# Kernel optimization log

Measured on AMD Instinct MI355X. Metric: run time of the kernel, lower is better.

## Reference

```python
import jax, jax.numpy as jnp
import numpy as np

N = 10000      # atoms
E = 160000     # edges (avg degree 16)
C = 64         # hidden_channels
R = 32         # num_rbf
CUTOFF = 5.0   # cutoff_upper (cutoff_lower = 0)


def setup_inputs() -> dict:
    key = jax.random.key(0)
    ks = jax.random.split(key, 12)
    X = jax.random.normal(ks[0], (N, C, 3, 3), jnp.float32) * 0.1
    edge_index = jax.random.randint(ks[1], (2, E), 0, N, dtype=jnp.int32)
    edge_weight = jax.random.uniform(ks[2], (E,), jnp.float32, minval=0.1, maxval=CUTOFF)
    edge_attr = jax.random.normal(ks[3], (E, R), jnp.float32)
    # scalar MLP: R -> C -> 2C -> 3C (weights stored [in, out] so y = x @ W + b)
    W_s1 = jax.random.normal(ks[4], (R, C), jnp.float32) / np.sqrt(R)
    b_s1 = jnp.zeros((C,), jnp.float32)
    W_s2 = jax.random.normal(ks[5], (C, 2 * C), jnp.float32) / np.sqrt(C)
    b_s2 = jnp.zeros((2 * C,), jnp.float32)
    W_s3 = jax.random.normal(ks[6], (2 * C, 3 * C), jnp.float32) / np.sqrt(2 * C)
    b_s3 = jnp.zeros((3 * C,), jnp.float32)
    # 6 channel-mixing linears (bias-free), stored [in, out]
    Wt = jax.random.normal(ks[7], (6, C, C), jnp.float32) / np.sqrt(C)
    return dict(X=X, edge_index=edge_index, edge_weight=edge_weight, edge_attr=edge_attr,
                W_s1=W_s1, b_s1=b_s1, W_s2=W_s2, b_s2=b_s2, W_s3=W_s3, b_s3=b_s3, Wt=Wt)


def _decompose(T):
    # irreducible decomposition of [..., 3, 3]
    eye = jnp.eye(3, dtype=T.dtype)
    I = (jnp.trace(T, axis1=-2, axis2=-1) / 3.0)[..., None, None] * eye
    A = 0.5 * (T - jnp.swapaxes(T, -2, -1))
    S = 0.5 * (T + jnp.swapaxes(T, -2, -1)) - I
    return I, A, S


def _tnorm(T):
    # Frobenius norm^2 over last two dims -> [..., C]
    return jnp.sum(T * T, axis=(-2, -1))


def _chan_lin(T, W):
    # linear over channel dim: [n, k, 3, 3] x [k, l] -> [n, l, 3, 3]
    return jnp.einsum('nkij,kl->nlij', T, W)


def reference(X, edge_index, edge_weight, edge_attr,
              W_s1, b_s1, W_s2, b_s2, W_s3, b_s3, Wt):
    act = jax.nn.silu
    # CosineCutoff with cutoff_lower == 0
    Cw = 0.5 * (jnp.cos(edge_weight * (jnp.pi / CUTOFF)) + 1.0)
    Cw = Cw * (edge_weight < CUTOFF).astype(X.dtype)

    # scalar edge MLP -> per-edge per-channel factors for I/A/S
    a = act(edge_attr @ W_s1 + b_s1)
    a = act(a @ W_s2 + b_s2)
    a = act(a @ W_s3 + b_s3)                       # [E, 3C]
    a = (a * Cw[:, None]).reshape(-1, C, 3)        # [E, C, 3]

    # normalize node tensors
    Xn = X / (_tnorm(X) + 1.0)[..., None, None]
    I, A, S = _decompose(Xn)
    I = _chan_lin(I, Wt[0])
    A = _chan_lin(A, Wt[1])
    S = _chan_lin(S, Wt[2])
    Y = I + A + S

    src, dst = edge_index[0], edge_index[1]

    def mp(factor, T):
        # gather -> weight -> scatter-add   factor: [E, C, 1, 1]
        msg = factor * T[dst]
        return jax.ops.segment_sum(msg, src, num_segments=N)

    msg = (mp(a[:, :, 0, None, None], I)
           + mp(a[:, :, 1, None, None], A)
           + mp(a[:, :, 2, None, None], S))

    # O(3) equivariance group
    M = jnp.matmul(msg, Y) + jnp.matmul(Y, msg)
    I2, A2, S2 = _decompose(M)
    normp1 = (_tnorm(I2 + A2 + S2) + 1.0)[..., None, None]
    I2 = _chan_lin(I2 / normp1, Wt[3])
    A2 = _chan_lin(A2 / normp1, Wt[4])
    S2 = _chan_lin(S2 / normp1, Wt[5])
    dX = I2 + A2 + S2
    return Xn + dX + jnp.matmul(dX, dX)
```

## Files before the change

kernel.cpp:

```cpp
#include <hip/hip_runtime.h>
#include <math.h>

#define C 64
#define R 32
#define CUTOFF 5.0f
#define PI_F 3.14159265358979323846f

typedef __attribute__((ext_vector_type(8))) short short8b;
typedef __attribute__((ext_vector_type(4))) short short4b;
typedef __attribute__((ext_vector_type(4))) float f32x4;

__device__ __forceinline__ float silu(float x) { return x / (1.0f + __expf(-x)); }

__device__ __forceinline__ unsigned short f2bfu(float x) {
  unsigned u = __builtin_bit_cast(unsigned, x);
  u += 0x7FFF + ((u >> 16) & 1);
  return (unsigned short)(u >> 16);
}
__device__ __forceinline__ float bflo(unsigned u) {
  return __builtin_bit_cast(float, u << 16);
}
__device__ __forceinline__ float bfhi(unsigned u) {
  return __builtin_bit_cast(float, u & 0xffff0000u);
}
__device__ __forceinline__ unsigned pk2(float a, float b) {
  return (unsigned)f2bfu(a) | ((unsigned)f2bfu(b) << 16);
}

__global__ __launch_bounds__(256) void k_misc(
    const int* __restrict__ ei, int* __restrict__ deg, int E, int histB,
    const float* __restrict__ W1, const float* __restrict__ W2,
    const float* __restrict__ W3, unsigned short* __restrict__ Wf,
    const float* __restrict__ X, const float* __restrict__ Wt,
    float* __restrict__ Xn, float* __restrict__ nf32,
    unsigned* __restrict__ nfh, int N) {
  __shared__ float comps[4][C][12];
  const int bid = blockIdx.x;
  if (bid < histB) {
    int e = bid * 256 + threadIdx.x;
    if (e < E) atomicAdd(&deg[ei[e]], 1);
    return;
  }
  if (bid < histB + 136) {
    int id = (bid - histB) * 256 + threadIdx.x;
    if (id >= 34816) return;
    int i, l, t;
    if (id < 2048) {
      i = id & 7; l = (id >> 3) & 63; t = id >> 9;
      int nt = t % 4, ks = t / 4;
      int k = ks * 32 + ((l >> 4) << 2) + (i & 3) + ((i >> 2) << 4);
      int n = nt * 16 + (l & 15);
      Wf[id] = f2bfu(W1[(size_t)k * 64 + n]);
    } else if (id < 10240) {
      int id2 = id - 2048;
      i = id2 & 7; l = (id2 >> 3) & 63; t = id2 >> 9;
      int nt = t % 8, ks = t / 8;
      int k = ks * 32 + ((l >> 4) << 2) + (i & 3) + ((i >> 2) << 4);
      int n = nt * 16 + (l & 15);
      Wf[id] = f2bfu(W2[(size_t)k * 128 + n]);
    } else {
      int id2 = id - 10240;
      i = id2 & 7; l = (id2 >> 3) & 63; t = id2 >> 9;
      int nt = t % 12, ks = t / 12;
      int k = ks * 32 + ((l >> 4) << 2) + (i & 3) + ((i >> 2) << 4);
      int nperm = nt * 16 + (l & 15);
      int norig = (nperm & 63) * 3 + (nperm >> 6);
      Wf[id] = f2bfu(W3[(size_t)k * 192 + norig]);
    }
    return;
  }
  const int ln = threadIdx.x >> 6;
  const int c  = threadIdx.x & 63;
  const int node = (bid - histB - 136) * 4 + ln;
  if (node < N) {
    const float* xp = X + ((size_t)node * C + c) * 9;
    float x[9]; float nrm = 0.f;
#pragma unroll
    for (int j = 0; j < 9; j++) { x[j] = xp[j]; nrm += x[j] * x[j]; }
    const float inv = 1.0f / (nrm + 1.0f);
#pragma unroll
    for (int j = 0; j < 9; j++) x[j] *= inv;
    float* xnp = Xn + (size_t)node * 576 + c;
#pragma unroll
    for (int j = 0; j < 9; j++) xnp[j * 64] = x[j];
    const float tr3 = (x[0] + x[4] + x[8]) * (1.f / 3.f);
    float* cp = comps[ln][c];
    cp[0] = tr3;
    cp[1] = 0.5f * (x[1] - x[3]);
    cp[2] = 0.5f * (x[2] - x[6]);
    cp[3] = 0.5f * (x[5] - x[7]);
    cp[4] = x[0] - tr3;
    cp[5] = x[4] - tr3;
    cp[6] = x[8] - tr3;
    cp[7] = 0.5f * (x[1] + x[3]);
    cp[8] = 0.5f * (x[2] + x[6]);
    cp[9] = 0.5f * (x[5] + x[7]);
  }
  __syncthreads();
  if (node < N) {
    const float* W0 = Wt;
    const float* Wt1 = Wt + C * C;
    const float* Wt2 = Wt + 2 * C * C;
    float o[10];
#pragma unroll
    for (int j = 0; j < 10; j++) o[j] = 0.f;
    for (int k = 0; k < C; k++) {
      const float w0 = W0[k * C + c];
      const float w1 = Wt1[k * C + c];
      const float w2 = Wt2[k * C + c];
      const float4* cq = (const float4*)comps[ln][k];
      float4 q0 = cq[0], q1 = cq[1];
      float2 q2 = *(const float2*)(comps[ln][k] + 8);
      o[0] += q0.x * w0;
      o[1] += q0.y * w1; o[2] += q0.z * w1; o[3] += q0.w * w1;
      o[4] += q1.x * w2; o[5] += q1.y * w2; o[6] += q1.z * w2;
      o[7] += q1.w * w2; o[8] += q2.x * w2; o[9] += q2.y * w2;
    }
    float* np_ = nf32 + (size_t)node * 768 + c * 12;
    *(float4*)np_       = make_float4(o[0], o[1], o[2], o[3]);
    *(float4*)(np_ + 4) = make_float4(o[4], o[5], o[6], o[7]);
    *(float4*)(np_ + 8) = make_float4(o[8], o[9], 0.f, 0.f);
    unsigned ui = f2bfu(o[0]);
    unsigned* hp = nfh + (size_t)node * 384 + c * 6;
    *(uint2*)hp       = make_uint2(ui | ((unsigned)f2bfu(o[4]) << 16),
                                   ui | ((unsigned)f2bfu(o[5]) << 16));
    *(uint2*)(hp + 2) = make_uint2(ui | ((unsigned)f2bfu(o[6]) << 16),
                                   pk2(o[1], o[7]));
    *(uint2*)(hp + 4) = make_uint2(pk2(o[2], o[8]), pk2(o[3], o[9]));
  }
}

__global__ __launch_bounds__(1024) void k_scan(const int* __restrict__ deg,
                                               int* __restrict__ off,
                                               int* __restrict__ cur, int N) {
  __shared__ int sums[1024];
  const int t = threadIdx.x;
  const int L = (N + 1023) / 1024;
  const int base = t * L;
  int s = 0;
  for (int j = 0; j < L; j++) if (base + j < N) s += deg[base + j];
  sums[t] = s;
  __syncthreads();
  for (int d = 1; d < 1024; d <<= 1) {
    int v = (t >= d) ? sums[t - d] : 0;
    __syncthreads();
    sums[t] += v;
    __syncthreads();
  }
  int run = (t > 0) ? sums[t - 1] : 0;
  for (int j = 0; j < L; j++) {
    int i = base + j;
    if (i < N) { off[i] = run; run += deg[i]; cur[i] = 0; }
  }
  if (t == 1023) off[N] = sums[1023];
}

__global__ __launch_bounds__(256) void k_mlp(
    const float* __restrict__ ew, const float* __restrict__ ea,
    const int* __restrict__ ei,
    const float* __restrict__ b1, const float* __restrict__ b2,
    const float* __restrict__ b3, const unsigned short* __restrict__ Wf,
    const int* __restrict__ off, int* __restrict__ cur,
    int* __restrict__ dlist, unsigned short* __restrict__ fa, int E) {
  __shared__ __align__(16) unsigned short attrB[64][40];
  __shared__ __align__(16) unsigned short h1B[64][72];
  __shared__ __align__(16) unsigned short h2B[64][136];
  __shared__ float cws[64];
  __shared__ int posB[64];
  const int tid = threadIdx.x;
  const int e0 = blockIdx.x * 64;

  {
    int el = tid >> 2, q = tid & 3;
    int e = e0 + el;
    uint4 pk = make_uint4(0, 0, 0, 0);
    if (e < E) {
      const float4* fp4 = (const float4*)(ea + (size_t)e * R + q * 8);
      float4 x0 = fp4[0], x1 = fp4[1];
      pk.x = pk2(x0.x, x0.y); pk.y = pk2(x0.z, x0.w);
      pk.z = pk2(x1.x, x1.y); pk.w = pk2(x1.z, x1.w);
    }
    *(uint4*)&attrB[el][q * 8] = pk;
  }
  if (tid < 64) {
    int e = e0 + tid;
    if (e < E) {
      float wgt = ew[e];
      float cc = 0.5f * (cosf(wgt * (PI_F / CUTOFF)) + 1.0f);
      cws[tid] = (wgt < CUTOFF) ? cc : 0.f;
      int s = ei[e];
      int d = ei[E + e];
      int pos = off[s] + atomicAdd(&cur[s], 1);
      posB[tid] = pos;
      dlist[pos] = d;
    } else {
      cws[tid] = 0.f;
      posB[tid] = 0;
    }
  }
  __syncthreads();

  const int wv = tid >> 6, l = tid & 63;
  const int g = l >> 4, r = l & 15;
  const short8b* WfL1 = (const short8b*)Wf;
  const short8b* WfL2 = WfL1 + 256;
  const short8b* WfL3 = WfL1 + 1280;

  {
    short8b w1f = WfL1[wv * 64 + l];
    float4 bb = *(const float4*)(b1 + wv * 16 + g * 4);
    f32x4 binit = (f32x4){bb.x, bb.y, bb.z, bb.w};
#pragma unroll
    for (int t = 0; t < 4; t++) {
      const unsigned short* arow = &attrB[t * 16 + r][0];
      short4b lo = *(const short4b*)(arow + g * 4);
      short4b hi = *(const short4b*)(arow + 16 + g * 4);
      short8b efrag = __builtin_shufflevector(lo, hi, 0, 1, 2, 3, 4, 5, 6, 7);
      f32x4 acc = binit;
      acc = __builtin_amdgcn_mfma_f32_16x16x32_bf16(w1f, efrag, acc, 0, 0, 0);
      uint2 v = make_uint2(pk2(silu(acc[0]), silu(acc[1])),
                           pk2(silu(acc[2]), silu(acc[3])));
      *(uint2*)&h1B[t * 16 + r][wv * 16 + g * 4] = v;
    }
  }
  __syncthreads();

  {
    short8b w2f[2][2];
#pragma unroll
    for (int ks = 0; ks < 2; ks++)
#pragma unroll
      for (int j = 0; j < 2; j++)
        w2f[ks][j] = WfL2[(ks * 8 + 2 * wv + j) * 64 + l];
    float4 bA = *(const float4*)(b2 + (2 * wv) * 16 + g * 4);
    float4 bB = *(const float4*)(b2 + (2 * wv + 1) * 16 + g * 4);
    f32x4 biA = (f32x4){bA.x, bA.y, bA.z, bA.w};
    f32x4 biB = (f32x4){bB.x, bB.y, bB.z, bB.w};
#pragma unroll
    for (int t = 0; t < 4; t++) {
      f32x4 aA = biA, aB = biB;
      const unsigned short* hrow = &h1B[t * 16 + r][0];
#pragma unroll
      for (int ks = 0; ks < 2; ks++) {
        short4b lo = *(const short4b*)(hrow + ks * 32 + g * 4);
        short4b hi = *(const short4b*)(hrow + ks * 32 + 16 + g * 4);
        short8b efrag = __builtin_shufflevector(lo, hi, 0, 1, 2, 3, 4, 5, 6, 7);
        aA = __builtin_amdgcn_mfma_f32_16x16x32_bf16(w2f[ks][0], efrag, aA, 0, 0, 0);
        aB = __builtin_amdgcn_mfma_f32_16x16x32_bf16(w2f[ks][1], efrag, aB, 0, 0, 0);
      }
      uint2 vA = make_uint2(pk2(silu(aA[0]), silu(aA[1])),
                            pk2(silu(aA[2]), silu(aA[3])));
      uint2 vB = make_uint2(pk2(silu(aB[0]), silu(aB[1])),
                            pk2(silu(aB[2]), silu(aB[3])));
      *(uint2*)&h2B[t * 16 + r][(2 * wv) * 16 + g * 4] = vA;
      *(uint2*)&h2B[t * 16 + r][(2 * wv + 1) * 16 + g * 4] = vB;
    }
  }
  __syncthreads();

  {
    short8b w3f[4][3];
#pragma unroll
    for (int ks = 0; ks < 4; ks++)
#pragma unroll
      for (int j = 0; j < 3; j++)
        w3f[ks][j] = WfL3[(ks * 12 + j * 4 + wv) * 64 + l];
    const int ch = wv * 16 + r;
    float bb0 = b3[ch * 3 + 0];
    float bb1 = b3[ch * 3 + 1];
    float bb2v = b3[ch * 3 + 2];
#pragma unroll
    for (int t = 0; t < 4; t++) {
      f32x4 p0v = (f32x4){bb0, bb0, bb0, bb0};
      f32x4 p1v = (f32x4){bb1, bb1, bb1, bb1};
      f32x4 p2v = (f32x4){bb2v, bb2v, bb2v, bb2v};
      const unsigned short* hrow = &h2B[t * 16 + r][0];
#pragma unroll
      for (int ks = 0; ks < 4; ks++) {
        short4b lo = *(const short4b*)(hrow + ks * 32 + g * 4);
        short4b hi = *(const short4b*)(hrow + ks * 32 + 16 + g * 4);
        short8b a = __builtin_shufflevector(lo, hi, 0, 1, 2, 3, 4, 5, 6, 7);
        p0v = __builtin_amdgcn_mfma_f32_16x16x32_bf16(a, w3f[ks][0], p0v, 0, 0, 0);
        p1v = __builtin_amdgcn_mfma_f32_16x16x32_bf16(a, w3f[ks][1], p1v, 0, 0, 0);
        p2v = __builtin_amdgcn_mfma_f32_16x16x32_bf16(a, w3f[ks][2], p2v, 0, 0, 0);
      }
#pragma unroll
      for (int reg = 0; reg < 4; reg++) {
        int el = t * 16 + g * 4 + reg;
        int e = e0 + el;
        float cw = cws[el];
        float s0 = silu(p0v[reg]) * cw;
        float s1 = silu(p1v[reg]) * cw;
        float s2 = silu(p2v[reg]) * cw;
        unsigned u2 = (unsigned)f2bfu(s2) << 16;
        uint2 v = make_uint2((unsigned)f2bfu(s0) | u2,
                             (unsigned)f2bfu(s1) | u2);
        if (e < E) {
          size_t pos = (size_t)posB[el];
          *(uint2*)((char*)fa + (pos << 9) + ch * 8) = v;
        }
      }
    }
  }
}

struct Slot { uint2 f, q0, q1, q2; };

__device__ __forceinline__ void load_slot(
    Slot& s, int ii, int t0, const int* __restrict__ dlist,
    const unsigned short* __restrict__ fa, const unsigned* __restrict__ nfh,
    int c) {
  if (ii < t0) {
    int d = dlist[ii];
    s.f = *(const uint2*)((const char*)fa + ((size_t)ii << 9) + (c << 3));
    const uint2* np = (const uint2*)(nfh + (size_t)d * 384 + c * 6);
    s.q0 = np[0]; s.q1 = np[1]; s.q2 = np[2];
  } else {
    s.f = make_uint2(0, 0); s.q0 = s.f; s.q1 = s.f; s.q2 = s.f;
  }
}

#define DOT2(ACC, A, B) \
  asm("v_dot2_f32_bf16 %0, %1, %2, %0" : "+v"(ACC) : "v"(A), "v"(B))

__device__ __forceinline__ void acc_slot(const Slot& s, float* m) {
  unsigned F02 = s.f.x;
  unsigned F12 = s.f.y;
  unsigned F12m = F12 ^ 0x8000u;
  DOT2(m[0], F02, s.q0.x);
  DOT2(m[4], F02, s.q0.y);
  DOT2(m[8], F02, s.q1.x);
  DOT2(m[1], F12,  s.q1.y);
  DOT2(m[3], F12m, s.q1.y);
  DOT2(m[2], F12,  s.q2.x);
  DOT2(m[6], F12m, s.q2.x);
  DOT2(m[5], F12,  s.q2.y);
  DOT2(m[7], F12m, s.q2.y);
}

__global__ __launch_bounds__(256) void k_gather_out(
    const int* __restrict__ dlist, const int* __restrict__ off,
    const unsigned short* __restrict__ fa, const unsigned* __restrict__ nfh,
    const float* __restrict__ nf32, const float* __restrict__ Xn,
    const float* __restrict__ Wt, float* __restrict__ out, int N) {
  const int wv = threadIdx.x >> 6;
  const int c  = threadIdx.x & 63;
  const int node = blockIdx.x;
  __shared__ float part[3][64][10];
  __shared__ float comps[64][12];

  float m[9];
#pragma unroll
  for (int j = 0; j < 9; j++) m[j] = 0.f;

  {
    const int t0 = off[node + 1];
    int p = off[node] + wv;
    if (p < t0) {
      Slot s0, s1, s2, s3;
      load_slot(s0, p,      t0, dlist, fa, nfh, c);
      load_slot(s1, p + 4,  t0, dlist, fa, nfh, c);
      load_slot(s2, p + 8,  t0, dlist, fa, nfh, c);
      load_slot(s3, p + 12, t0, dlist, fa, nfh, c);
      p += 16;
      while (p < t0) {
        acc_slot(s0, m); load_slot(s0, p,      t0, dlist, fa, nfh, c);
        acc_slot(s1, m); load_slot(s1, p + 4,  t0, dlist, fa, nfh, c);
        acc_slot(s2, m); load_slot(s2, p + 8,  t0, dlist, fa, nfh, c);
        acc_slot(s3, m); load_slot(s3, p + 12, t0, dlist, fa, nfh, c);
        p += 16;
      }
      acc_slot(s0, m); acc_slot(s1, m); acc_slot(s2, m); acc_slot(s3, m);
    }
  }
  if (wv > 0) {
#pragma unroll
    for (int j = 0; j < 9; j++) part[wv - 1][c][j] = m[j];
  }
  __syncthreads();

  if (wv == 0) {
#pragma unroll
    for (int j = 0; j < 9; j++)
      m[j] += part[0][c][j] + part[1][c][j] + part[2][c][j];
    const float* p = nf32 + (size_t)node * 768 + c * 12;
    float4 q0 = *(const float4*)p;
    float4 q1 = *(const float4*)(p + 4);
    float2 q2 = *(const float2*)(p + 8);
    float iv = q0.x, a0 = q0.y, a1 = q0.z, a2 = q0.w;
    float s00 = q1.x, s11 = q1.y, s22 = q1.z, s01 = q1.w;
    float s02 = q2.x, s12 = q2.y;
    float Y[9] = { iv + s00, a0 + s01, a1 + s02,
                   s01 - a0, iv + s11, a2 + s12,
                   s02 - a1, s12 - a2, iv + s22 };
    float M[9];
#pragma unroll
    for (int i2 = 0; i2 < 3; i2++)
#pragma unroll
      for (int j2 = 0; j2 < 3; j2++) {
        float acc = 0.f;
#pragma unroll
        for (int k2 = 0; k2 < 3; k2++)
          acc += m[i2 * 3 + k2] * Y[k2 * 3 + j2] + Y[i2 * 3 + k2] * m[k2 * 3 + j2];
        M[i2 * 3 + j2] = acc;
      }
    float nrm = 0.f;
#pragma unroll
    for (int j = 0; j < 9; j++) nrm += M[j] * M[j];
    const float inv = 1.0f / (nrm + 1.0f);
    const float tr3 = (M[0] + M[4] + M[8]) * (1.f / 3.f);
    float* cp = comps[c];
    cp[0] = tr3 * inv;
    cp[1] = 0.5f * (M[1] - M[3]) * inv;
    cp[2] = 0.5f * (M[2] - M[6]) * inv;
    cp[3] = 0.5f * (M[5] - M[7]) * inv;
    cp[4] = (M[0] - tr3) * inv;
    cp[5] = (M[4] - tr3) * inv;
    cp[6] = (M[8] - tr3) * inv;
    cp[7] = 0.5f * (M[1] + M[3]) * inv;
    cp[8] = 0.5f * (M[2] + M[6]) * inv;
    cp[9] = 0.5f * (M[5] + M[7]) * inv;
  }
  __syncthreads();

  float o[10];
#pragma unroll
  for (int j = 0; j < 10; j++) o[j] = 0.f;
  {
    const float* W3p = Wt + 3 * C * C;
    const float* W4p = Wt + 4 * C * C;
    const float* W5p = Wt + 5 * C * C;
    for (int k = wv * 16; k < wv * 16 + 16; k++) {
      const float w3 = W3p[k * C + c];
      const float w4 = W4p[k * C + c];
      const float w5 = W5p[k * C + c];
      const float4* cq = (const float4*)comps[k];
      float4 q0 = cq[0], q1 = cq[1];
      float2 q2 = *(const float2*)(comps[k] + 8);
      o[0] += q0.x * w3;
      o[1] += q0.y * w4; o[2] += q0.z * w4; o[3] += q0.w * w4;
      o[4] += q1.x * w5; o[5] += q1.y * w5; o[6] += q1.z * w5;
      o[7] += q1.w * w5; o[8] += q2.x * w5; o[9] += q2.y * w5;
    }
  }
  if (wv > 0) {
#pragma unroll
    for (int j = 0; j < 10; j++) part[wv - 1][c][j] = o[j];
  }
  __syncthreads();
  if (wv == 0) {
#pragma unroll
    for (int j = 0; j < 10; j++)
      o[j] += part[0][c][j] + part[1][c][j] + part[2][c][j];
    float dX[9] = { o[0] + o[4], o[1] + o[7], o[2] + o[8],
                    o[7] - o[1], o[0] + o[5], o[3] + o[9],
                    o[8] - o[2], o[9] - o[3], o[0] + o[6] };
    float dd[9];
#pragma unroll
    for (int i2 = 0; i2 < 3; i2++)
#pragma unroll
      for (int j2 = 0; j2 < 3; j2++) {
        float acc = 0.f;
#pragma unroll
        for (int k2 = 0; k2 < 3; k2++) acc += dX[i2 * 3 + k2] * dX[k2 * 3 + j2];
        dd[i2 * 3 + j2] = acc;
      }
    const float* xnp = Xn + (size_t)node * 576 + c;
    float* op = out + ((size_t)node * C + c) * 9;
#pragma unroll
    for (int j = 0; j < 9; j++) op[j] = xnp[j * 64] + dX[j] + dd[j];
  }
}

extern "C" void kernel_launch(void* const* d_in, const int* in_sizes, int n_in,
                              void* d_out, int out_size, void* d_ws, size_t ws_size,
                              hipStream_t stream) {
  const float* X  = (const float*)d_in[0];
  const int*   ei = (const int*)d_in[1];
  const float* ew = (const float*)d_in[2];
  const float* ea = (const float*)d_in[3];
  const float* W1 = (const float*)d_in[4];
  const float* b1 = (const float*)d_in[5];
  const float* W2 = (const float*)d_in[6];
  const float* b2 = (const float*)d_in[7];
  const float* W3 = (const float*)d_in[8];
  const float* b3 = (const float*)d_in[9];
  const float* Wt = (const float*)d_in[10];
  const int N = in_sizes[0] / (C * 9);
  const int E = in_sizes[1] / 2;

  float* nf32 = (float*)d_ws;
  float* Xn   = nf32 + (size_t)N * 768;
  unsigned* nfh = (unsigned*)(Xn + (size_t)N * 576);
  unsigned short* fa = (unsigned short*)(nfh + (size_t)N * 384);
  unsigned short* Wf = fa + (size_t)E * 256;
  int* deg  = (int*)(Wf + 34816);
  int* off  = deg + N;
  int* cur  = off + N + 1;
  int* dlist = cur + N;

  const int histB = (E + 255) / 256;
  const int nodeB = (N + 3) / 4;
  (void)hipMemsetAsync(deg, 0, (size_t)N * sizeof(int), stream);
  k_misc<<<histB + 136 + nodeB, 256, 0, stream>>>(ei, deg, E, histB,
                                                  W1, W2, W3, Wf,
                                                  X, Wt, Xn, nf32, nfh, N);
  k_scan<<<1, 1024, 0, stream>>>(deg, off, cur, N);
  k_mlp<<<(E + 63) / 64, 256, 0, stream>>>(ew, ea, ei, b1, b2, b3, Wf,
                                           off, cur, dlist, fa, E);
  k_gather_out<<<N, 256, 0, stream>>>(dlist, off, fa, nfh, nf32, Xn, Wt,
                                      (float*)d_out, N);
}
```

Before: 171.3 us.

## Move node transform into MLP kernel and use hardware bf16 pack conversion

Moves the per-node normalize, decompose and channel-mix work out of the histogram/weight-prep kernel and into the edge-MLP launch as extra blocks sharing one smem buffer. This shortens the kernel that precedes the serial single-block scan and lets the node work run alongside the MLP. The h1/h2 shared-memory row strides are padded to reduce bank conflicts. Software float-to-bf16 rounding is replaced with the v_cvt_pk_bf16_f32 instruction. The cost is a larger shared-memory footprint per block for the merged kernel, which may lower occupancy, and the hardware conversion's rounding could differ slightly from the software version.

```diff
diff --git a/kernel.cpp b/kernel.cpp
--- a/kernel.cpp
+++ b/kernel.cpp
@@ -17,116 +17,46 @@
   u += 0x7FFF + ((u >> 16) & 1);
   return (unsigned short)(u >> 16);
 }
-__device__ __forceinline__ float bflo(unsigned u) {
-  return __builtin_bit_cast(float, u << 16);
-}
-__device__ __forceinline__ float bfhi(unsigned u) {
-  return __builtin_bit_cast(float, u & 0xffff0000u);
-}
-__device__ __forceinline__ unsigned pk2(float a, float b) {
-  return (unsigned)f2bfu(a) | ((unsigned)f2bfu(b) << 16);
+__device__ __forceinline__ unsigned pk2c(float a, float b) {
+  unsigned r;
+  asm("v_cvt_pk_bf16_f32 %0, %1, %2" : "=v"(r) : "v"(a), "v"(b));
+  return r;
 }
 
 __global__ __launch_bounds__(256) void k_misc(
     const int* __restrict__ ei, int* __restrict__ deg, int E, int histB,
     const float* __restrict__ W1, const float* __restrict__ W2,
-    const float* __restrict__ W3, unsigned short* __restrict__ Wf,
-    const float* __restrict__ X, const float* __restrict__ Wt,
-    float* __restrict__ Xn, float* __restrict__ nf32,
-    unsigned* __restrict__ nfh, int N) {
-  __shared__ float comps[4][C][12];
+    const float* __restrict__ W3, unsigned short* __restrict__ Wf) {
   const int bid = blockIdx.x;
   if (bid < histB) {
     int e = bid * 256 + threadIdx.x;
     if (e < E) atomicAdd(&deg[ei[e]], 1);
     return;
   }
-  if (bid < histB + 136) {
-    int id = (bid - histB) * 256 + threadIdx.x;
-    if (id >= 34816) return;
-    int i, l, t;
-    if (id < 2048) {
-      i = id & 7; l = (id >> 3) & 63; t = id >> 9;
-      int nt = t % 4, ks = t / 4;
-      int k = ks * 32 + ((l >> 4) << 2) + (i & 3) + ((i >> 2) << 4);
-      int n = nt * 16 + (l & 15);
-      Wf[id] = f2bfu(W1[(size_t)k * 64 + n]);
-    } else if (id < 10240) {
-      int id2 = id - 2048;
-      i = id2 & 7; l = (id2 >> 3) & 63; t = id2 >> 9;
-      int nt = t % 8, ks = t / 8;
-      int k = ks * 32 + ((l >> 4) << 2) + (i & 3) + ((i >> 2) << 4);
-      int n = nt * 16 + (l & 15);
-      Wf[id] = f2bfu(W2[(size_t)k * 128 + n]);
-    } else {
-      int id2 = id - 10240;
-      i = id2 & 7; l = (id2 >> 3) & 63; t = id2 >> 9;
-      int nt = t % 12, ks = t / 12;
-      int k = ks * 32 + ((l >> 4) << 2) + (i & 3) + ((i >> 2) << 4);
-      int nperm = nt * 16 + (l & 15);
-      int norig = (nperm & 63) * 3 + (nperm >> 6);
-      Wf[id] = f2bfu(W3[(size_t)k * 192 + norig]);
-    }
-    return;
-  }
-  const int ln = threadIdx.x >> 6;
-  const int c  = threadIdx.x & 63;
-  const int node = (bid - histB - 136) * 4 + ln;
-  if (node < N) {
-    const float* xp = X + ((size_t)node * C + c) * 9;
-    float x[9]; float nrm = 0.f;
-#pragma unroll
-    for (int j = 0; j < 9; j++) { x[j] = xp[j]; nrm += x[j] * x[j]; }
-    const float inv = 1.0f / (nrm + 1.0f);
-#pragma unroll
-    for (int j = 0; j < 9; j++) x[j] *= inv;
-    float* xnp = Xn + (size_t)node * 576 + c;
-#pragma unroll
-    for (int j = 0; j < 9; j++) xnp[j * 64] = x[j];
-    const float tr3 = (x[0] + x[4] + x[8]) * (1.f / 3.f);
-    float* cp = comps[ln][c];
-    cp[0] = tr3;
-    cp[1] = 0.5f * (x[1] - x[3]);
-    cp[2] = 0.5f * (x[2] - x[6]);
-    cp[3] = 0.5f * (x[5] - x[7]);
-    cp[4] = x[0] - tr3;
-    cp[5] = x[4] - tr3;
-    cp[6] = x[8] - tr3;
-    cp[7] = 0.5f * (x[1] + x[3]);
-    cp[8] = 0.5f * (x[2] + x[6]);
-    cp[9] = 0.5f * (x[5] + x[7]);
-  }
-  __syncthreads();
-  if (node < N) {
-    const float* W0 = Wt;
-    const float* Wt1 = Wt + C * C;
-    const float* Wt2 = Wt + 2 * C * C;
-    float o[10];
-#pragma unroll
-    for (int j = 0; j < 10; j++) o[j] = 0.f;
-    for (int k = 0; k < C; k++) {
-      const float w0 = W0[k * C + c];
-      const float w1 = Wt1[k * C + c];
-      const float w2 = Wt2[k * C + c];
-      const float4* cq = (const float4*)comps[ln][k];
-      float4 q0 = cq[0], q1 = cq[1];
-      float2 q2 = *(const float2*)(comps[ln][k] + 8);
-      o[0] += q0.x * w0;
-      o[1] += q0.y * w1; o[2] += q0.z * w1; o[3] += q0.w * w1;
-      o[4] += q1.x * w2; o[5] += q1.y * w2; o[6] += q1.z * w2;
-      o[7] += q1.w * w2; o[8] += q2.x * w2; o[9] += q2.y * w2;
-    }
-    float* np_ = nf32 + (size_t)node * 768 + c * 12;
-    *(float4*)np_       = make_float4(o[0], o[1], o[2], o[3]);
-    *(float4*)(np_ + 4) = make_float4(o[4], o[5], o[6], o[7]);
-    *(float4*)(np_ + 8) = make_float4(o[8], o[9], 0.f, 0.f);
-    unsigned ui = f2bfu(o[0]);
-    unsigned* hp = nfh + (size_t)node * 384 + c * 6;
-    *(uint2*)hp       = make_uint2(ui | ((unsigned)f2bfu(o[4]) << 16),
-                                   ui | ((unsigned)f2bfu(o[5]) << 16));
-    *(uint2*)(hp + 2) = make_uint2(ui | ((unsigned)f2bfu(o[6]) << 16),
-                                   pk2(o[1], o[7]));
-    *(uint2*)(hp + 4) = make_uint2(pk2(o[2], o[8]), pk2(o[3], o[9]));
+  int id = (bid - histB) * 256 + threadIdx.x;
+  if (id >= 34816) return;
+  int i, l, t;
+  if (id < 2048) {
+    i = id & 7; l = (id >> 3) & 63; t = id >> 9;
+    int nt = t % 4, ks = t / 4;
+    int k = ks * 32 + ((l >> 4) << 2) + (i & 3) + ((i >> 2) << 4);
+    int n = nt * 16 + (l & 15);
+    Wf[id] = f2bfu(W1[(size_t)k * 64 + n]);
+  } else if (id < 10240) {
+    int id2 = id - 2048;
+    i = id2 & 7; l = (id2 >> 3) & 63; t = id2 >> 9;
+    int nt = t % 8, ks = t / 8;
+    int k = ks * 32 + ((l >> 4) << 2) + (i & 3) + ((i >> 2) << 4);
+    int n = nt * 16 + (l & 15);
+    Wf[id] = f2bfu(W2[(size_t)k * 128 + n]);
+  } else {
+    int id2 = id - 10240;
+    i = id2 & 7; l = (id2 >> 3) & 63; t = id2 >> 9;
+    int nt = t % 12, ks = t / 12;
+    int k = ks * 32 + ((l >> 4) << 2) + (i & 3) + ((i >> 2) << 4);
+    int nperm = nt * 16 + (l & 15);
+    int norig = (nperm & 63) * 3 + (nperm >> 6);
+    Wf[id] = f2bfu(W3[(size_t)k * 192 + norig]);
   }
 }
 
@@ -155,19 +85,85 @@
   if (t == 1023) off[N] = sums[1023];
 }
 
-__global__ __launch_bounds__(256) void k_mlp(
+__global__ __launch_bounds__(256) void k_mega(
     const float* __restrict__ ew, const float* __restrict__ ea,
     const int* __restrict__ ei,
     const float* __restrict__ b1, const float* __restrict__ b2,
     const float* __restrict__ b3, const unsigned short* __restrict__ Wf,
     const int* __restrict__ off, int* __restrict__ cur,
-    int* __restrict__ dlist, unsigned short* __restrict__ fa, int E) {
-  __shared__ __align__(16) unsigned short attrB[64][40];
-  __shared__ __align__(16) unsigned short h1B[64][72];
-  __shared__ __align__(16) unsigned short h2B[64][136];
+    int* __restrict__ dlist, unsigned short* __restrict__ fa, int E, int mlpB,
+    const float* __restrict__ X, const float* __restrict__ Wt,
+    float* __restrict__ Xn, float* __restrict__ nf32,
+    unsigned* __restrict__ nfh, int N) {
+  __shared__ __align__(16) char smem[32768];
   __shared__ float cws[64];
   __shared__ int posB[64];
   const int tid = threadIdx.x;
+
+  if ((int)blockIdx.x >= mlpB) {
+    float (*comps)[C][12] = (float (*)[C][12])smem;
+    const int ln = tid >> 6;
+    const int c  = tid & 63;
+    const int node = ((int)blockIdx.x - mlpB) * 4 + ln;
+    if (node < N) {
+      const float* xp = X + ((size_t)node * C + c) * 9;
+      float x[9]; float nrm = 0.f;
+#pragma unroll
+      for (int j = 0; j < 9; j++) { x[j] = xp[j]; nrm += x[j] * x[j]; }
+      const float inv = 1.0f / (nrm + 1.0f);
+#pragma unroll
+      for (int j = 0; j < 9; j++) x[j] *= inv;
+      float* xnp = Xn + (size_t)node * 576 + c;
+#pragma unroll
+      for (int j = 0; j < 9; j++) xnp[j * 64] = x[j];
+      const float tr3 = (x[0] + x[4] + x[8]) * (1.f / 3.f);
+      float* cp = comps[ln][c];
+      cp[0] = tr3;
+      cp[1] = 0.5f * (x[1] - x[3]);
+      cp[2] = 0.5f * (x[2] - x[6]);
+      cp[3] = 0.5f * (x[5] - x[7]);
+      cp[4] = x[0] - tr3;
+      cp[5] = x[4] - tr3;
+      cp[6] = x[8] - tr3;
+      cp[7] = 0.5f * (x[1] + x[3]);
+      cp[8] = 0.5f * (x[2] + x[6]);
+      cp[9] = 0.5f * (x[5] + x[7]);
+    }
+    __syncthreads();
+    if (node < N) {
+      const float* W0 = Wt;
+      const float* Wt1 = Wt + C * C;
+      const float* Wt2 = Wt + 2 * C * C;
+      float o[10];
+#pragma unroll
+      for (int j = 0; j < 10; j++) o[j] = 0.f;
+      for (int k = 0; k < C; k++) {
+        const float w0 = W0[k * C + c];
+        const float w1 = Wt1[k * C + c];
+        const float w2 = Wt2[k * C + c];
+        const float4* cq = (const float4*)comps[ln][k];
+        float4 q0 = cq[0], q1 = cq[1];
+        float2 q2 = *(const float2*)(comps[ln][k] + 8);
+        o[0] += q0.x * w0;
+        o[1] += q0.y * w1; o[2] += q0.z * w1; o[3] += q0.w * w1;
+        o[4] += q1.x * w2; o[5] += q1.y * w2; o[6] += q1.z * w2;
+        o[7] += q1.w * w2; o[8] += q2.x * w2; o[9] += q2.y * w2;
+      }
+      float* np_ = nf32 + (size_t)node * 768 + c * 12;
+      *(float4*)np_       = make_float4(o[0], o[1], o[2], o[3]);
+      *(float4*)(np_ + 4) = make_float4(o[4], o[5], o[6], o[7]);
+      *(float4*)(np_ + 8) = make_float4(o[8], o[9], 0.f, 0.f);
+      unsigned* hp = nfh + (size_t)node * 384 + c * 6;
+      *(uint2*)hp       = make_uint2(pk2c(o[0], o[4]), pk2c(o[0], o[5]));
+      *(uint2*)(hp + 2) = make_uint2(pk2c(o[0], o[6]), pk2c(o[1], o[7]));
+      *(uint2*)(hp + 4) = make_uint2(pk2c(o[2], o[8]), pk2c(o[3], o[9]));
+    }
+    return;
+  }
+
+  unsigned short (*attrB)[40]  = (unsigned short (*)[40])smem;
+  unsigned short (*h1B)[76]    = (unsigned short (*)[76])(smem + 5120);
+  unsigned short (*h2B)[140]   = (unsigned short (*)[140])(smem + 14848);
   const int e0 = blockIdx.x * 64;
 
   {
@@ -177,8 +173,8 @@
     if (e < E) {
       const float4* fp4 = (const float4*)(ea + (size_t)e * R + q * 8);
       float4 x0 = fp4[0], x1 = fp4[1];
-      pk.x = pk2(x0.x, x0.y); pk.y = pk2(x0.z, x0.w);
-      pk.z = pk2(x1.x, x1.y); pk.w = pk2(x1.z, x1.w);
+      pk.x = pk2c(x0.x, x0.y); pk.y = pk2c(x0.z, x0.w);
+      pk.z = pk2c(x1.x, x1.y); pk.w = pk2c(x1.z, x1.w);
     }
     *(uint4*)&attrB[el][q * 8] = pk;
   }
@@ -218,8 +214,8 @@
       short8b efrag = __builtin_shufflevector(lo, hi, 0, 1, 2, 3, 4, 5, 6, 7);
       f32x4 acc = binit;
       acc = __builtin_amdgcn_mfma_f32_16x16x32_bf16(w1f, efrag, acc, 0, 0, 0);
-      uint2 v = make_uint2(pk2(silu(acc[0]), silu(acc[1])),
-                           pk2(silu(acc[2]), silu(acc[3])));
+      uint2 v = make_uint2(pk2c(silu(acc[0]), silu(acc[1])),
+                           pk2c(silu(acc[2]), silu(acc[3])));
       *(uint2*)&h1B[t * 16 + r][wv * 16 + g * 4] = v;
     }
   }
@@ -248,10 +244,10 @@
         aA = __builtin_amdgcn_mfma_f32_16x16x32_bf16(w2f[ks][0], efrag, aA, 0, 0, 0);
         aB = __builtin_amdgcn_mfma_f32_16x16x32_bf16(w2f[ks][1], efrag, aB, 0, 0, 0);
       }
-      uint2 vA = make_uint2(pk2(silu(aA[0]), silu(aA[1])),
-                            pk2(silu(aA[2]), silu(aA[3])));
-      uint2 vB = make_uint2(pk2(silu(aB[0]), silu(aB[1])),
-                            pk2(silu(aB[2]), silu(aB[3])));
+      uint2 vA = make_uint2(pk2c(silu(aA[0]), silu(aA[1])),
+                            pk2c(silu(aA[2]), silu(aA[3])));
+      uint2 vB = make_uint2(pk2c(silu(aB[0]), silu(aB[1])),
+                            pk2c(silu(aB[2]), silu(aB[3])));
       *(uint2*)&h2B[t * 16 + r][(2 * wv) * 16 + g * 4] = vA;
       *(uint2*)&h2B[t * 16 + r][(2 * wv + 1) * 16 + g * 4] = vB;
     }
@@ -292,9 +288,7 @@
         float s0 = silu(p0v[reg]) * cw;
         float s1 = silu(p1v[reg]) * cw;
         float s2 = silu(p2v[reg]) * cw;
-        unsigned u2 = (unsigned)f2bfu(s2) << 16;
-        uint2 v = make_uint2((unsigned)f2bfu(s0) | u2,
-                             (unsigned)f2bfu(s1) | u2);
+        uint2 v = make_uint2(pk2c(s0, s2), pk2c(s1, s2));
         if (e < E) {
           size_t pos = (size_t)posB[el];
           *(uint2*)((char*)fa + (pos << 9) + ch * 8) = v;
@@ -500,14 +494,14 @@
   int* dlist = cur + N;
 
   const int histB = (E + 255) / 256;
+  const int mlpB  = (E + 63) / 64;
   const int nodeB = (N + 3) / 4;
   (void)hipMemsetAsync(deg, 0, (size_t)N * sizeof(int), stream);
-  k_misc<<<histB + 136 + nodeB, 256, 0, stream>>>(ei, deg, E, histB,
-                                                  W1, W2, W3, Wf,
-                                                  X, Wt, Xn, nf32, nfh, N);
+  k_misc<<<histB + 136, 256, 0, stream>>>(ei, deg, E, histB, W1, W2, W3, Wf);
   k_scan<<<1, 1024, 0, stream>>>(deg, off, cur, N);
-  k_mlp<<<(E + 63) / 64, 256, 0, stream>>>(ew, ea, ei, b1, b2, b3, Wf,
-                                           off, cur, dlist, fa, E);
+  k_mega<<<mlpB + nodeB, 256, 0, stream>>>(ew, ea, ei, b1, b2, b3, Wf,
+                                           off, cur, dlist, fa, E, mlpB,
+                                           X, Wt, Xn, nf32, nfh, N);
   k_gather_out<<<N, 256, 0, stream>>>(dlist, off, fa, nfh, nf32, Xn, Wt,
                                       (float*)d_out, N);
 }
```

Result: faster. 161.5 us (-5.7%).
